# Kernel tuning notes

Hardware: AMD Instinct MI355X
Metric: run time of the kernel (lower is better)

The kernel has to match this reference:

```python
import jax, jax.numpy as jnp
import numpy as np

B, L, T, D = 4, 256, 256, 512
NEG_INF = -1e30


def setup_inputs() -> dict:
    key = jax.random.key(0)
    ks = jax.random.split(key, 8)
    x = jax.random.normal(ks[0], (B, L, D), dtype=jnp.float32)
    memory = jax.random.normal(ks[1], (B, T, D), dtype=jnp.float32)
    memory_mask = jnp.ones((B, T), dtype=jnp.int32)
    scale = 1.0 / np.sqrt(D)
    W1 = jax.random.normal(ks[2], (D, D), dtype=jnp.float32) * scale
    b1 = jnp.zeros((D,), dtype=jnp.float32)
    W2 = jax.random.normal(ks[3], (D, D), dtype=jnp.float32) * scale
    b2 = jnp.zeros((D,), dtype=jnp.float32)
    wt = jax.random.normal(ks[4], (D,), dtype=jnp.float32) * scale
    bt = jnp.zeros((), dtype=jnp.float32)
    return {"x": x, "memory": memory, "W1": W1, "b1": b1, "W2": W2,
            "b2": b2, "wt": wt, "bt": bt, "memory_mask": memory_mask}


def reference(x, memory, W1, b1, W2, b2, wt, bt, memory_mask):
    # item1: [B,L,D], item2: [B,T,D]
    item1 = jnp.einsum('bld,ed->ble', x, W1) + b1
    item2 = jnp.einsum('btd,ed->bte', memory, W2) + b2
    # additive (Bahdanau) score: tanh of broadcast sum, then GEMV with wt -> [B,L,T]
    item = jnp.tanh(item1[:, :, None, :] + item2[:, None, :, :])  # [B,L,T,D]
    S = jnp.einsum('bltd,d->blt', item, wt) + bt
    # memory mask: [B,1,T]
    valid = (memory_mask[:, None, :] != 0)
    # direction == 'forward': keep t >= l (upper triangular incl. diagonal)
    fwd_mask = jnp.triu(jnp.ones((L, T), dtype=bool))
    S = jnp.where(valid & fwd_mask[None, :, :], S, NEG_INF)
    P = jax.nn.softmax(S, axis=-1)  # dropout p=0.0 -> identity
    return jnp.einsum('blt,btd->bld', P, memory)
```

## Files before the change

### kernel.cpp

```cpp
#include <hip/hip_runtime.h>
#include <math.h>

#define BB 4
#define LL 256
#define TT 256
#define DD 512

#define EXP2K 2.885390081777927f

using short8  = __attribute__((ext_vector_type(8))) short;
using f32x4   = __attribute__((ext_vector_type(4))) float;

__device__ __forceinline__ unsigned cvt2bf(float a, float b) {
  unsigned r;
  asm("v_cvt_pk_bf16_f32 %0, %1, %2" : "=v"(r) : "v"(a), "v"(b));
  return r;
}

__global__ __launch_bounds__(256) void proj_gemm(
    const float* __restrict__ x, const float* __restrict__ mem,
    const float* __restrict__ W1, const float* __restrict__ b1,
    const float* __restrict__ W2, const float* __restrict__ b2,
    float* __restrict__ E1, float* __restrict__ E2c)
{
  __shared__ __align__(16) char Abuf[32 * 144];
  __shared__ __align__(16) char Bbuf[64 * 144];

  const int tid = threadIdx.x;
  const int m0 = blockIdx.x * 32;
  const int n0 = blockIdx.y * 64;
  const bool second = (m0 >= BB * LL);

  const float* A    = second ? mem + (size_t)(m0 - BB * LL) * DD
                             : x   + (size_t)m0 * DD;
  const float* W    = second ? W2 : W1;
  const float* bias = second ? b2 : b1;

  const int srow = tid >> 4;
  const int kq   = (tid & 15) * 4;

  const int lane = tid & 63;
  const int wid  = tid >> 6;
  const int r0   = (wid & 1) * 16;
  const int n0w  = (wid >> 1) * 32;
  const int lr   = lane & 15;
  const int lg   = lane >> 4;

  const int aoff  = (r0 + lr) * 144 + lg * 16;
  const int boff0 = (n0w + lr) * 144 + lg * 16;
  const int boff1 = (n0w + 16 + lr) * 144 + lg * 16;

  f32x4 acc0 = {0.f, 0.f, 0.f, 0.f};
  f32x4 acc1 = {0.f, 0.f, 0.f, 0.f};

  const float* Ap = A + (size_t)srow * DD + kq;
  const float* Wp = W + (size_t)(n0 + srow) * DD + kq;

  float4 rA0 = *(const float4*)(Ap);
  float4 rA1 = *(const float4*)(Ap + (size_t)16 * DD);
  float4 rB0 = *(const float4*)(Wp);
  float4 rB1 = *(const float4*)(Wp + (size_t)16 * DD);
  float4 rB2 = *(const float4*)(Wp + (size_t)32 * DD);
  float4 rB3 = *(const float4*)(Wp + (size_t)48 * DD);

  for (int kc = 0; kc < DD; kc += 64) {
    __syncthreads();
    {
      uint2 u0 = {cvt2bf(rA0.x, rA0.y), cvt2bf(rA0.z, rA0.w)};
      *(uint2*)(Abuf + srow * 144 + kq * 2) = u0;
      uint2 u1 = {cvt2bf(rA1.x, rA1.y), cvt2bf(rA1.z, rA1.w)};
      *(uint2*)(Abuf + (srow + 16) * 144 + kq * 2) = u1;
      uint2 v0 = {cvt2bf(rB0.x, rB0.y), cvt2bf(rB0.z, rB0.w)};
      *(uint2*)(Bbuf + srow * 144 + kq * 2) = v0;
      uint2 v1 = {cvt2bf(rB1.x, rB1.y), cvt2bf(rB1.z, rB1.w)};
      *(uint2*)(Bbuf + (srow + 16) * 144 + kq * 2) = v1;
      uint2 v2 = {cvt2bf(rB2.x, rB2.y), cvt2bf(rB2.z, rB2.w)};
      *(uint2*)(Bbuf + (srow + 32) * 144 + kq * 2) = v2;
      uint2 v3 = {cvt2bf(rB3.x, rB3.y), cvt2bf(rB3.z, rB3.w)};
      *(uint2*)(Bbuf + (srow + 48) * 144 + kq * 2) = v3;
    }
    __syncthreads();
    if (kc + 64 < DD) {
      const float* An = Ap + kc + 64;
      const float* Wn = Wp + kc + 64;
      rA0 = *(const float4*)(An);
      rA1 = *(const float4*)(An + (size_t)16 * DD);
      rB0 = *(const float4*)(Wn);
      rB1 = *(const float4*)(Wn + (size_t)16 * DD);
      rB2 = *(const float4*)(Wn + (size_t)32 * DD);
      rB3 = *(const float4*)(Wn + (size_t)48 * DD);
    }
#pragma unroll
    for (int ks = 0; ks < 2; ++ks) {
      short8 af  = *(const short8*)(Abuf + aoff  + ks * 64);
      short8 bf0 = *(const short8*)(Bbuf + boff0 + ks * 64);
      short8 bf1 = *(const short8*)(Bbuf + boff1 + ks * 64);
      acc0 = __builtin_amdgcn_mfma_f32_16x16x32_bf16(af, bf0, acc0, 0, 0, 0);
      acc1 = __builtin_amdgcn_mfma_f32_16x16x32_bf16(af, bf1, acc1, 0, 0, 0);
    }
  }

#pragma unroll
  for (int nf = 0; nf < 2; ++nf) {
    const f32x4 a = nf ? acc1 : acc0;
    const int col = n0 + n0w + nf * 16 + lr;
    const float bv = bias[col];
#pragma unroll
    for (int i = 0; i < 4; ++i) {
      const int mrow = m0 + r0 + lg * 4 + i;
      const float val = exp2f((a[i] + bv) * EXP2K);
      if (!second) {
        E1[(size_t)mrow * DD + col] = val;
      } else {
        const int m2 = mrow - BB * LL;
        E2c[((size_t)(col >> 2) * (BB * TT) + m2) * 4 + (col & 3)] = val;
      }
    }
  }
}

__global__ __launch_bounds__(512) void score_softmax(
    const float* __restrict__ E1, const float* __restrict__ E2c,
    const float* __restrict__ wt, const int* __restrict__ mask,
    float* __restrict__ Pg)
{
  __shared__ float prt[2][4][8][64];
  __shared__ float S[2][TT];

  const int tid = threadIdx.x;
  const int tl  = tid & 63;
  const int wv  = tid >> 6;
  const int dq  = __builtin_amdgcn_readfirstlane(wv);

  const int bid = blockIdx.x;
  const int k   = bid & 7;
  const int b   = k >> 1;
  const int lp  = (bid >> 3) + ((k & 1) << 6);

  const int r0 = lp;
  const int r1 = 255 - lp;
  const int tc0 = r0 >> 6;
  const int tc1 = r1 >> 6;

  const size_t strE2 = (size_t)(BB * TT);
  const float4* wp  = (const float4*)wt + dq * 16;
  const float4* q0p = (const float4*)(E1 + (size_t)(b * LL + r0) * DD) + dq * 16;
  const float4* q1p = (const float4*)(E1 + (size_t)(b * LL + r1) * DD) + dq * 16;

  for (int tc = tc0; tc < 4; ++tc) {
    const bool shr = (tc >= tc1);
    const int t = tc * 64 + tl;
    const float4* vp = (const float4*)E2c + (size_t)(dq * 16) * strE2 + (b * TT + t);

    float a0 = 0.f, a1 = 0.f, a2 = 0.f, a3 = 0.f;
    float b0 = 0.f, b1 = 0.f, b2 = 0.f, b3 = 0.f;
    if (shr) {
#pragma unroll 8
      for (int j = 0; j < 16; ++j) {
        float4 vv = vp[(size_t)j * strE2];
        float4 q0 = q0p[j];
        float4 q1 = q1p[j];
        float4 w  = wp[j];
        a0 = fmaf(w.x, __builtin_amdgcn_rcpf(fmaf(q0.x, vv.x, 1.0f)), a0);
        a1 = fmaf(w.y, __builtin_amdgcn_rcpf(fmaf(q0.y, vv.y, 1.0f)), a1);
        a2 = fmaf(w.z, __builtin_amdgcn_rcpf(fmaf(q0.z, vv.z, 1.0f)), a2);
        a3 = fmaf(w.w, __builtin_amdgcn_rcpf(fmaf(q0.w, vv.w, 1.0f)), a3);
        b0 = fmaf(w.x, __builtin_amdgcn_rcpf(fmaf(q1.x, vv.x, 1.0f)), b0);
        b1 = fmaf(w.y, __builtin_amdgcn_rcpf(fmaf(q1.y, vv.y, 1.0f)), b1);
        b2 = fmaf(w.z, __builtin_amdgcn_rcpf(fmaf(q1.z, vv.z, 1.0f)), b2);
        b3 = fmaf(w.w, __builtin_amdgcn_rcpf(fmaf(q1.w, vv.w, 1.0f)), b3);
      }
    } else {
#pragma unroll 8
      for (int j = 0; j < 16; ++j) {
        float4 vv = vp[(size_t)j * strE2];
        float4 q0 = q0p[j];
        float4 w  = wp[j];
        a0 = fmaf(w.x, __builtin_amdgcn_rcpf(fmaf(q0.x, vv.x, 1.0f)), a0);
        a1 = fmaf(w.y, __builtin_amdgcn_rcpf(fmaf(q0.y, vv.y, 1.0f)), a1);
        a2 = fmaf(w.z, __builtin_amdgcn_rcpf(fmaf(q0.z, vv.z, 1.0f)), a2);
        a3 = fmaf(w.w, __builtin_amdgcn_rcpf(fmaf(q0.w, vv.w, 1.0f)), a3);
      }
    }
    prt[0][tc][dq][tl] = (a0 + a1) + (a2 + a3);
    if (shr) prt[1][tc][dq][tl] = (b0 + b1) + (b2 + b3);
  }
  __syncthreads();

  {
    const int rr = tid >> 8;
    const int t  = tid & 255;
    const int lo = (rr ? tc1 : tc0) << 6;
    if (t >= lo) {
      const float* pp = &prt[rr][t >> 6][0][t & 63];
      float s = 0.f;
#pragma unroll
      for (int oc = 0; oc < 8; ++oc) s += pp[oc * 64];
      S[rr][t] = s;
    } else {
      S[rr][t] = 5e29f;
    }
  }
  __syncthreads();

  if (wv < 2) {
    const int row = wv ? r1 : r0;
    const int tb = tl * 4;
    float4 h = *(const float4*)(&S[wv][tb]);
    const int4 mk = *(const int4*)(mask + b * TT + tb);
    float v0 = (tb + 0 >= row && mk.x != 0) ? -2.0f * h.x : -1e30f;
    float v1 = (tb + 1 >= row && mk.y != 0) ? -2.0f * h.y : -1e30f;
    float v2 = (tb + 2 >= row && mk.z != 0) ? -2.0f * h.z : -1e30f;
    float v3 = (tb + 3 >= row && mk.w != 0) ? -2.0f * h.w : -1e30f;
    float mx = fmaxf(fmaxf(v0, v1), fmaxf(v2, v3));
#pragma unroll
    for (int o = 1; o < 64; o <<= 1) mx = fmaxf(mx, __shfl_xor(mx, o));
    float e0 = __expf(v0 - mx), e1 = __expf(v1 - mx),
          e2 = __expf(v2 - mx), e3 = __expf(v3 - mx);
    float sm = (e0 + e1) + (e2 + e3);
#pragma unroll
    for (int o = 1; o < 64; o <<= 1) sm += __shfl_xor(sm, o);
    const float rinv = 1.0f / sm;
    float4 pv = {e0 * rinv, e1 * rinv, e2 * rinv, e3 * rinv};
    *(float4*)(Pg + (size_t)(b * LL + row) * TT + tb) = pv;
  }
}

__global__ __launch_bounds__(256) void pv_gemm(
    const float* __restrict__ Pg, const float* __restrict__ mem,
    float* __restrict__ out)
{
  __shared__ __align__(16) char Abuf[32 * 144];
  __shared__ __align__(16) char Bbuf[64 * 144];

  const int tid = threadIdx.x;
  const int bid = blockIdx.x;
  const int b   = bid >> 6;
  const int rem = bid & 63;
  const int m0  = (rem >> 3) * 32;
  const int n0  = (rem & 7) * 64;

  const int arow = tid >> 3;
  const int k8   = (tid & 7) * 8;
  const int nq   = tid & 15;
  const int kp0  = tid >> 4;

  const int lane = tid & 63;
  const int wid  = tid >> 6;
  const int r0   = (wid & 1) * 16;
  const int n0w  = (wid >> 1) * 32;
  const int lr   = lane & 15;
  const int lg   = lane >> 4;

  const int aoff  = (r0 + lr) * 144 + lg * 16;
  const int boff0 = (n0w + lr) * 144 + lg * 16;
  const int boff1 = (n0w + 16 + lr) * 144 + lg * 16;

  f32x4 acc0 = {0.f, 0.f, 0.f, 0.f};
  f32x4 acc1 = {0.f, 0.f, 0.f, 0.f};

  const float* Pb = Pg + (size_t)(b * LL) * TT;
  const float* Mb = mem + (size_t)(b * TT) * DD;
  const float* Pa = Pb + (size_t)(m0 + arow) * TT + k8;
  const float* Mq = Mb + n0 + nq * 4;

  float4 pa1 = *(const float4*)(Pa);
  float4 pa2 = *(const float4*)(Pa + 4);
  float4 fa0 = *(const float4*)(Mq + (size_t)(kp0 * 2) * DD);
  float4 fb0 = *(const float4*)(Mq + (size_t)(kp0 * 2 + 1) * DD);
  float4 fa1 = *(const float4*)(Mq + (size_t)((kp0 + 16) * 2) * DD);
  float4 fb1 = *(const float4*)(Mq + (size_t)((kp0 + 16) * 2 + 1) * DD);

  for (int kc = 0; kc < TT; kc += 64) {
    __syncthreads();
    {
      uint4 u = {cvt2bf(pa1.x, pa1.y), cvt2bf(pa1.z, pa1.w),
                 cvt2bf(pa2.x, pa2.y), cvt2bf(pa2.z, pa2.w)};
      *(uint4*)(Abuf + arow * 144 + k8 * 2) = u;
    }
    {
      *(unsigned*)(Bbuf + (nq * 4 + 0) * 144 + kp0 * 4) = cvt2bf(fa0.x, fb0.x);
      *(unsigned*)(Bbuf + (nq * 4 + 1) * 144 + kp0 * 4) = cvt2bf(fa0.y, fb0.y);
      *(unsigned*)(Bbuf + (nq * 4 + 2) * 144 + kp0 * 4) = cvt2bf(fa0.z, fb0.z);
      *(unsigned*)(Bbuf + (nq * 4 + 3) * 144 + kp0 * 4) = cvt2bf(fa0.w, fb0.w);
      const int kp1 = kp0 + 16;
      *(unsigned*)(Bbuf + (nq * 4 + 0) * 144 + kp1 * 4) = cvt2bf(fa1.x, fb1.x);
      *(unsigned*)(Bbuf + (nq * 4 + 1) * 144 + kp1 * 4) = cvt2bf(fa1.y, fb1.y);
      *(unsigned*)(Bbuf + (nq * 4 + 2) * 144 + kp1 * 4) = cvt2bf(fa1.z, fb1.z);
      *(unsigned*)(Bbuf + (nq * 4 + 3) * 144 + kp1 * 4) = cvt2bf(fa1.w, fb1.w);
    }
    __syncthreads();
    if (kc + 64 < TT) {
      const int kn = kc + 64;
      pa1 = *(const float4*)(Pa + kn);
      pa2 = *(const float4*)(Pa + kn + 4);
      fa0 = *(const float4*)(Mq + (size_t)(kn + kp0 * 2) * DD);
      fb0 = *(const float4*)(Mq + (size_t)(kn + kp0 * 2 + 1) * DD);
      fa1 = *(const float4*)(Mq + (size_t)(kn + (kp0 + 16) * 2) * DD);
      fb1 = *(const float4*)(Mq + (size_t)(kn + (kp0 + 16) * 2 + 1) * DD);
    }
#pragma unroll
    for (int ks = 0; ks < 2; ++ks) {
      short8 af  = *(const short8*)(Abuf + aoff  + ks * 64);
      short8 bf0 = *(const short8*)(Bbuf + boff0 + ks * 64);
      short8 bf1 = *(const short8*)(Bbuf + boff1 + ks * 64);
      acc0 = __builtin_amdgcn_mfma_f32_16x16x32_bf16(af, bf0, acc0, 0, 0, 0);
      acc1 = __builtin_amdgcn_mfma_f32_16x16x32_bf16(af, bf1, acc1, 0, 0, 0);
    }
  }

#pragma unroll
  for (int nf = 0; nf < 2; ++nf) {
    const f32x4 a = nf ? acc1 : acc0;
    const int col = n0 + n0w + nf * 16 + lr;
#pragma unroll
    for (int i = 0; i < 4; ++i) {
      const int mrow = m0 + r0 + lg * 4 + i;
      out[(size_t)(b * LL + mrow) * DD + col] = a[i];
    }
  }
}

extern "C" void kernel_launch(void* const* d_in, const int* in_sizes, int n_in,
                              void* d_out, int out_size, void* d_ws, size_t ws_size,
                              hipStream_t stream) {
  const float* x   = (const float*)d_in[0];
  const float* mem = (const float*)d_in[1];
  const float* W1  = (const float*)d_in[2];
  const float* b1  = (const float*)d_in[3];
  const float* W2  = (const float*)d_in[4];
  const float* b2  = (const float*)d_in[5];
  const float* wt  = (const float*)d_in[6];
  const int* mask  = (const int*)d_in[8];
  float* outp = (float*)d_out;

  float* E1  = (float*)d_ws;
  float* E2c = E1 + (size_t)BB * LL * DD;
  float* Pg  = E2c + (size_t)BB * TT * DD;

  proj_gemm<<<dim3((BB * LL + BB * TT) / 32, DD / 64), 256, 0, stream>>>(
      x, mem, W1, b1, W2, b2, E1, E2c);
  score_softmax<<<512, 512, 0, stream>>>(E1, E2c, wt, mask, Pg);
  pv_gemm<<<256, 256, 0, stream>>>(Pg, mem, outp);
}
```

Measured before the change: 32.69 us.

## Process four query rows per block in score kernel with 1024 threads

```diff
diff --git a/kernel.cpp b/kernel.cpp
--- a/kernel.cpp
+++ b/kernel.cpp
@@ -119,13 +119,19 @@
   }
 }
 
-__global__ __launch_bounds__(512) void score_softmax(
+#define SROW(r, q)                                                            \
+  a##r##0 = fmaf(w.x, __builtin_amdgcn_rcpf(fmaf(q.x, vv.x, 1.0f)), a##r##0); \
+  a##r##1 = fmaf(w.y, __builtin_amdgcn_rcpf(fmaf(q.y, vv.y, 1.0f)), a##r##1); \
+  a##r##2 = fmaf(w.z, __builtin_amdgcn_rcpf(fmaf(q.z, vv.z, 1.0f)), a##r##2); \
+  a##r##3 = fmaf(w.w, __builtin_amdgcn_rcpf(fmaf(q.w, vv.w, 1.0f)), a##r##3)
+
+__global__ __launch_bounds__(1024) void score_softmax(
     const float* __restrict__ E1, const float* __restrict__ E2c,
     const float* __restrict__ wt, const int* __restrict__ mask,
     float* __restrict__ Pg)
 {
-  __shared__ float prt[2][4][8][64];
-  __shared__ float S[2][TT];
+  __shared__ float prt[4][4][16][64];
+  __shared__ float S[4][TT];
 
   const int tid = threadIdx.x;
   const int tl  = tid & 63;
@@ -135,67 +141,54 @@
   const int bid = blockIdx.x;
   const int k   = bid & 7;
   const int b   = k >> 1;
-  const int lp  = (bid >> 3) + ((k & 1) << 6);
+  const int lp  = (bid >> 3) + ((k & 1) << 5);
 
   const int r0 = lp;
-  const int r1 = 255 - lp;
-  const int tc0 = r0 >> 6;
-  const int tc1 = r1 >> 6;
+  const int r1 = 127 - lp;
+  const int r2 = 128 + lp;
+  const int r3 = 255 - lp;
 
   const size_t strE2 = (size_t)(BB * TT);
-  const float4* wp  = (const float4*)wt + dq * 16;
-  const float4* q0p = (const float4*)(E1 + (size_t)(b * LL + r0) * DD) + dq * 16;
-  const float4* q1p = (const float4*)(E1 + (size_t)(b * LL + r1) * DD) + dq * 16;
-
-  for (int tc = tc0; tc < 4; ++tc) {
-    const bool shr = (tc >= tc1);
+  const float4* wp  = (const float4*)wt + dq * 8;
+  const float4* q0p = (const float4*)(E1 + (size_t)(b * LL + r0) * DD) + dq * 8;
+  const float4* q1p = (const float4*)(E1 + (size_t)(b * LL + r1) * DD) + dq * 8;
+  const float4* q2p = (const float4*)(E1 + (size_t)(b * LL + r2) * DD) + dq * 8;
+  const float4* q3p = (const float4*)(E1 + (size_t)(b * LL + r3) * DD) + dq * 8;
+
+#pragma unroll
+  for (int tc = 0; tc < 4; ++tc) {
     const int t = tc * 64 + tl;
-    const float4* vp = (const float4*)E2c + (size_t)(dq * 16) * strE2 + (b * TT + t);
-
-    float a0 = 0.f, a1 = 0.f, a2 = 0.f, a3 = 0.f;
-    float b0 = 0.f, b1 = 0.f, b2 = 0.f, b3 = 0.f;
-    if (shr) {
-#pragma unroll 8
-      for (int j = 0; j < 16; ++j) {
-        float4 vv = vp[(size_t)j * strE2];
-        float4 q0 = q0p[j];
-        float4 q1 = q1p[j];
-        float4 w  = wp[j];
-        a0 = fmaf(w.x, __builtin_amdgcn_rcpf(fmaf(q0.x, vv.x, 1.0f)), a0);
-        a1 = fmaf(w.y, __builtin_amdgcn_rcpf(fmaf(q0.y, vv.y, 1.0f)), a1);
-        a2 = fmaf(w.z, __builtin_amdgcn_rcpf(fmaf(q0.z, vv.z, 1.0f)), a2);
-        a3 = fmaf(w.w, __builtin_amdgcn_rcpf(fmaf(q0.w, vv.w, 1.0f)), a3);
-        b0 = fmaf(w.x, __builtin_amdgcn_rcpf(fmaf(q1.x, vv.x, 1.0f)), b0);
-        b1 = fmaf(w.y, __builtin_amdgcn_rcpf(fmaf(q1.y, vv.y, 1.0f)), b1);
-        b2 = fmaf(w.z, __builtin_amdgcn_rcpf(fmaf(q1.z, vv.z, 1.0f)), b2);
-        b3 = fmaf(w.w, __builtin_amdgcn_rcpf(fmaf(q1.w, vv.w, 1.0f)), b3);
-      }
-    } else {
-#pragma unroll 8
-      for (int j = 0; j < 16; ++j) {
-        float4 vv = vp[(size_t)j * strE2];
-        float4 q0 = q0p[j];
-        float4 w  = wp[j];
-        a0 = fmaf(w.x, __builtin_amdgcn_rcpf(fmaf(q0.x, vv.x, 1.0f)), a0);
-        a1 = fmaf(w.y, __builtin_amdgcn_rcpf(fmaf(q0.y, vv.y, 1.0f)), a1);
-        a2 = fmaf(w.z, __builtin_amdgcn_rcpf(fmaf(q0.z, vv.z, 1.0f)), a2);
-        a3 = fmaf(w.w, __builtin_amdgcn_rcpf(fmaf(q0.w, vv.w, 1.0f)), a3);
-      }
-    }
-    prt[0][tc][dq][tl] = (a0 + a1) + (a2 + a3);
-    if (shr) prt[1][tc][dq][tl] = (b0 + b1) + (b2 + b3);
+    const float4* vp = (const float4*)E2c + (size_t)(dq * 8) * strE2 + (b * TT + t);
+
+    float a00=0,a01=0,a02=0,a03=0;
+    float a10=0,a11=0,a12=0,a13=0;
+    float a20=0,a21=0,a22=0,a23=0;
+    float a30=0,a31=0,a32=0,a33=0;
+#pragma unroll
+    for (int j = 0; j < 8; ++j) {
+      const float4 vv = vp[(size_t)j * strE2];
+      const float4 w  = wp[j];
+      const float4 q0 = q0p[j];
+      SROW(0, q0);
+      if (tc >= 1) { const float4 q1 = q1p[j]; SROW(1, q1); }
+      if (tc >= 2) { const float4 q2 = q2p[j]; SROW(2, q2); }
+      if (tc >= 3) { const float4 q3 = q3p[j]; SROW(3, q3); }
+    }
+    prt[0][tc][dq][tl] = (a00 + a01) + (a02 + a03);
+    if (tc >= 1) prt[1][tc][dq][tl] = (a10 + a11) + (a12 + a13);
+    if (tc >= 2) prt[2][tc][dq][tl] = (a20 + a21) + (a22 + a23);
+    if (tc >= 3) prt[3][tc][dq][tl] = (a30 + a31) + (a32 + a33);
   }
   __syncthreads();
 
   {
     const int rr = tid >> 8;
     const int t  = tid & 255;
-    const int lo = (rr ? tc1 : tc0) << 6;
-    if (t >= lo) {
+    if ((t >> 6) >= rr) {
       const float* pp = &prt[rr][t >> 6][0][t & 63];
       float s = 0.f;
 #pragma unroll
-      for (int oc = 0; oc < 8; ++oc) s += pp[oc * 64];
+      for (int oc = 0; oc < 16; ++oc) s += pp[oc * 64];
       S[rr][t] = s;
     } else {
       S[rr][t] = 5e29f;
@@ -203,8 +196,8 @@
   }
   __syncthreads();
 
-  if (wv < 2) {
-    const int row = wv ? r1 : r0;
+  if (wv < 4) {
+    const int row = (wv & 2) ? ((wv & 1) ? r3 : r2) : ((wv & 1) ? r1 : r0);
     const int tb = tl * 4;
     float4 h = *(const float4*)(&S[wv][tb]);
     const int4 mk = *(const int4*)(mask + b * TT + tb);
@@ -340,6 +333,6 @@
 
   proj_gemm<<<dim3((BB * LL + BB * TT) / 32, DD / 64), 256, 0, stream>>>(
       x, mem, W1, b1, W2, b2, E1, E2c);
-  score_softmax<<<512, 512, 0, stream>>>(E1, E2c, wt, mask, Pg);
+  score_softmax<<<256, 1024, 0, stream>>>(E1, E2c, wt, mask, Pg);
   pv_gemm<<<256, 256, 0, stream>>>(Pg, mem, outp);
 }
```

Result: slower. 38.35 us (+17.3%).
